# Kernel tuning notes

Measured on AMD Instinct MI355X. Metric: run time of the kernel, lower is better.

## Reference

```python
import jax, jax.numpy as jnp
import numpy as np

D = 1024
H = 16
FF = 4096
B = 8
N = 1024


def layer_norm(x, w, b, eps=1e-5):
    mu = jnp.mean(x, axis=-1, keepdims=True)
    var = jnp.var(x, axis=-1, keepdims=True)
    return (x - mu) * jax.lax.rsqrt(var + eps) * w + b


def setup_inputs() -> dict:
    key = jax.random.key(0)
    ks = jax.random.split(key, 8)
    s = 1.0 / np.sqrt(D)
    return {
        "x": jax.random.normal(ks[0], (B, N, D), dtype=jnp.float32),
        "attention_ids": jax.random.randint(ks[1], (B, N), 0, 2, dtype=jnp.int32),
        "norm1_w": jnp.ones((D,), jnp.float32),
        "norm1_b": jnp.zeros((D,), jnp.float32),
        "proj_in_w": jax.random.normal(ks[2], (3 * D, D), dtype=jnp.float32) * s,
        "proj_out_w": jax.random.normal(ks[3], (D, D), dtype=jnp.float32) * s,
        "proj_out_b": jnp.zeros((D,), jnp.float32),
        "norm2_w": jnp.ones((D,), jnp.float32),
        "norm2_b": jnp.zeros((D,), jnp.float32),
        "lin1_w": jax.random.normal(ks[4], (FF, D), dtype=jnp.float32) * s,
        "lin1_b": jnp.zeros((FF,), jnp.float32),
        "lin2_w": jax.random.normal(ks[5], (D, FF), dtype=jnp.float32) * (1.0 / np.sqrt(FF)),
        "lin2_b": jnp.zeros((D,), jnp.float32),
    }


def reference(x, attention_ids, norm1_w, norm1_b, proj_in_w, proj_out_w, proj_out_b,
              norm2_w, norm2_b, lin1_w, lin1_b, lin2_w, lin2_b):
    bs, ns, d = x.shape
    dh = d // H
    scale = dh ** -0.5

    # norm1 then attention with residual on the NORMED x (as in source)
    xn = layer_norm(x, norm1_w, norm1_b)
    qkv = jnp.einsum("bnd,ed->bne", xn, proj_in_w)          # [b,n,3d]
    qkv = qkv.reshape(bs, ns, 3, H, dh).transpose(2, 0, 3, 1, 4)
    q, k, v = qkv[0], qkv[1], qkv[2]                         # [b,h,n,dh]
    attn = jnp.einsum("bhqd,bhkd->bhqk", q, k)               # [b,h,n,n]
    mask_bias = (attention_ids.astype(x.dtype) * -1e9)[:, None, None, :]
    attn = jax.nn.softmax((attn + mask_bias) * scale, axis=-1)
    o = jnp.einsum("bhqk,bhkd->bhqd", attn, v)
    o = o.transpose(0, 2, 1, 3).reshape(bs, ns, d)
    o = jnp.einsum("bnd,ed->bne", o, proj_out_w) + proj_out_b
    x1 = o + xn

    # norm2 then FFN with residual on the NORMED x
    x2 = layer_norm(x1, norm2_w, norm2_b)
    h = jax.nn.gelu(jnp.einsum("bnd,fd->bnf", x2, lin1_w) + lin1_b, approximate=False)
    y = jnp.einsum("bnf,df->bnd", h, lin2_w) + lin2_b
    return y + x2
```

## Files before the change

kernel.cpp:

```cpp
#include <hip/hip_runtime.h>
#include <hip/hip_bf16.h>

#define B_ 8
#define N_ 1024
#define D_ 1024
#define H_ 16
#define FF_ 4096
#define TOK_ (B_*N_)

typedef __attribute__((ext_vector_type(8))) short bf16x8;
typedef __attribute__((ext_vector_type(4))) float f32x4;

typedef const __attribute__((address_space(1))) void* gc_ptr;
typedef __attribute__((address_space(3))) void* lp_ptr;

__device__ __forceinline__ short f2bf(float f) {
    unsigned u = __builtin_bit_cast(unsigned, f);
    u = (u + 0x7FFFu + ((u >> 16) & 1u)) >> 16;
    return (short)u;
}

__global__ __launch_bounds__(256)
void cvt_bf16(const float* __restrict__ in, short* __restrict__ outp) {
    const size_t i = ((size_t)blockIdx.x * 256 + threadIdx.x) * 4;
    const float4 v = *(const float4*)(in + i);
    short4 o;
    o.x = f2bf(v.x); o.y = f2bf(v.y); o.z = f2bf(v.z); o.w = f2bf(v.w);
    *(short4*)(outp + i) = o;
}

__global__ __launch_bounds__(256)
void ln_kernel(const float* __restrict__ in, const float* __restrict__ w,
               const float* __restrict__ bi, float* __restrict__ o32,
               short* __restrict__ obf) {
    const int row = blockIdx.x;
    const int tid = threadIdx.x;
    const float4 v = ((const float4*)(in + (size_t)row * D_))[tid];
    float s = v.x + v.y + v.z + v.w;
    float q = v.x * v.x + v.y * v.y + v.z * v.z + v.w * v.w;
#pragma unroll
    for (int off = 1; off < 64; off <<= 1) {
        s += __shfl_xor(s, off);
        q += __shfl_xor(q, off);
    }
    __shared__ float ss[4], sq[4];
    const int wave = tid >> 6, lane = tid & 63;
    if (lane == 0) { ss[wave] = s; sq[wave] = q; }
    __syncthreads();
    s = ss[0] + ss[1] + ss[2] + ss[3];
    q = sq[0] + sq[1] + sq[2] + sq[3];
    const float mu = s * (1.f / D_);
    const float var = q * (1.f / D_) - mu * mu;
    const float rs = rsqrtf(var + 1e-5f);
    const float4 wv = ((const float4*)w)[tid];
    const float4 bv = ((const float4*)bi)[tid];
    float4 o;
    o.x = (v.x - mu) * rs * wv.x + bv.x;
    o.y = (v.y - mu) * rs * wv.y + bv.y;
    o.z = (v.z - mu) * rs * wv.z + bv.z;
    o.w = (v.w - mu) * rs * wv.w + bv.w;
    ((float4*)(o32 + (size_t)row * D_))[tid] = o;
    short4 ob;
    ob.x = f2bf(o.x); ob.y = f2bf(o.y); ob.z = f2bf(o.z); ob.w = f2bf(o.w);
    *(short4*)(obf + (size_t)row * D_ + tid * 4) = ob;
}

template<int MODE>
__global__ __launch_bounds__(256, 2)
void gemm_bt(const short* __restrict__ A, const short* __restrict__ Bw,
             const float* __restrict__ bias, const float* __restrict__ res,
             void* __restrict__ outp, int M, int Nc, int K) {
    const int tid  = threadIdx.x;
    const int wave = tid >> 6;
    const int lane = tid & 63;
    const int m16  = lane & 15;
    const int quad = lane >> 4;
    const int wrow = (wave >> 1) * 64;
    const int wcol = (wave & 1) * 64;
    const int rowBase = blockIdx.y * 128;
    const int colBase = blockIdx.x * 128;

    __shared__ short sA[128 * 32];
    __shared__ short sB[128 * 32];

    f32x4 acc[4][4];
#pragma unroll
    for (int i = 0; i < 4; ++i)
#pragma unroll
        for (int j = 0; j < 4; ++j)
            acc[i][j] = {0.f, 0.f, 0.f, 0.f};

    const int r16 = lane >> 2;
    const int c4  = lane & 3;

    for (int kt = 0; kt < K; kt += 32) {
#pragma unroll
        for (int rep = 0; rep < 2; ++rep) {
            const int tr = rep * 64 + wave * 16;
            const short* ga = A  + (size_t)(rowBase + tr + r16) * K + kt + c4 * 8;
            const short* gb = Bw + (size_t)(colBase + tr + r16) * K + kt + c4 * 8;
            __builtin_amdgcn_global_load_lds((gc_ptr)ga, (lp_ptr)(sA + tr * 32), 16, 0, 0);
            __builtin_amdgcn_global_load_lds((gc_ptr)gb, (lp_ptr)(sB + tr * 32), 16, 0, 0);
        }
        asm volatile("s_waitcnt vmcnt(0)" ::: "memory");
        __syncthreads();

        bf16x8 af[4], bfr[4];
#pragma unroll
        for (int i = 0; i < 4; ++i)
            af[i] = *(const bf16x8*)(sA + (wrow + i * 16 + m16) * 32 + quad * 8);
#pragma unroll
        for (int j = 0; j < 4; ++j)
            bfr[j] = *(const bf16x8*)(sB + (wcol + j * 16 + m16) * 32 + quad * 8);
#pragma unroll
        for (int i = 0; i < 4; ++i)
#pragma unroll
            for (int j = 0; j < 4; ++j)
                acc[i][j] = __builtin_amdgcn_mfma_f32_16x16x32_bf16(af[i], bfr[j], acc[i][j], 0, 0, 0);
        __syncthreads();
    }

#pragma unroll
    for (int i = 0; i < 4; ++i) {
#pragma unroll
        for (int j = 0; j < 4; ++j) {
            const int col = colBase + wcol + j * 16 + m16;
#pragma unroll
            for (int r = 0; r < 4; ++r) {
                const int row = rowBase + wrow + i * 16 + quad * 4 + r;
                const float val = acc[i][j][r];
                if (MODE == 0) {
                    const int ci = col >> 10, hh = (col >> 6) & 15, dd = col & 63;
                    const int bb = row >> 10, nn = row & 1023;
                    size_t idx;
                    if (ci == 2)
                        idx = (size_t)2 * ((size_t)TOK_ * 1024) +
                              ((size_t)((bb * H_ + hh) * 64 + dd)) * N_ + nn;
                    else
                        idx = (size_t)ci * ((size_t)TOK_ * 1024) +
                              ((size_t)((bb * H_ + hh) * N_ + nn)) * 64 + dd;
                    ((short*)outp)[idx] = f2bf(val);
                } else if (MODE == 1) {
                    ((float*)outp)[(size_t)row * Nc + col] =
                        val + bias[col] + res[(size_t)row * Nc + col];
                } else {
                    const float t = val + bias[col];
                    const float g = 0.5f * t * (1.f + erff(t * 0.70710678118654752f));
                    ((short*)outp)[(size_t)row * Nc + col] = f2bf(g);
                }
            }
        }
    }
}

__global__ __launch_bounds__(256, 4)
void attn_kernel(const short* __restrict__ q, const short* __restrict__ k,
                 const short* __restrict__ vT, const int* __restrict__ ids,
                 short* __restrict__ outp) {
    const int tid  = threadIdx.x;
    const int wave = tid >> 6;
    const int lane = tid & 63;
    const int m    = lane & 15;
    const int quad = lane >> 4;
    const int b  = blockIdx.z;
    const int h  = blockIdx.y;
    const int q0 = blockIdx.x * 64;
    const size_t bh = ((size_t)b * H_ + h) * N_;

    __shared__ short Kb[2][4096];
    __shared__ short Vb[2][4096];
    __shared__ short Pl[4][16 * 40];

    const short* kbase  = k  + bh * 64;
    const short* vtbase = vT + bh * 64;
    const int* idrow = ids + b * N_;

    bf16x8 aq0, aq1;
    {
        const short* qp = q + (bh + q0 + wave * 16 + m) * 64;
        aq0 = *(const bf16x8*)(qp + quad * 8);
        aq1 = *(const bf16x8*)(qp + 32 + quad * 8);
    }

    const int l4 = lane >> 2, c3 = lane & 3;

    auto stage = [&](int t) {
        short* Kd = Kb[t & 1];
        short* Vd = Vb[t & 1];
        const int kt = t * 64;
        const int keyrow = 16 * wave + l4;
#pragma unroll
        for (int hh = 0; hh < 2; ++hh) {
            const short* gk = kbase + (size_t)(kt + keyrow) * 64 + hh * 32 + c3 * 8;
            __builtin_amdgcn_global_load_lds((gc_ptr)gk,
                (lp_ptr)(Kd + hh * 2048 + 512 * wave + lane * 8), 16, 0, 0);
        }
#pragma unroll
        for (int g = 0; g < 2; ++g) {
            const short* gv = vtbase + (size_t)keyrow * N_ + kt + g * 32 + c3 * 8;
            __builtin_amdgcn_global_load_lds((gc_ptr)gv,
                (lp_ptr)(Vd + g * 2048 + 512 * wave + lane * 8), 16, 0, 0);
        }
    };

    float plocal[4] = {0.f, 0.f, 0.f, 0.f};
    f32x4 o[4];
#pragma unroll
    for (int j = 0; j < 4; ++j) o[j] = {0.f, 0.f, 0.f, 0.f};

    short* pw = Pl[wave];

    stage(0);
    for (int t = 0; t < 16; ++t) {
        __syncthreads();
        if (t < 15) stage(t + 1);
        const short* Ks = Kb[t & 1];
        const short* Vs = Vb[t & 1];
        const int kt = t * 64;
#pragma unroll
        for (int g = 0; g < 2; ++g) {
            const float msk0 = -1e9f * (float)idrow[kt + g * 32 + m];
            const float msk1 = -1e9f * (float)idrow[kt + g * 32 + 16 + m];
            const bf16x8 b00 = *(const bf16x8*)(Ks + (g * 32 + m) * 32 + quad * 8);
            const bf16x8 b01 = *(const bf16x8*)(Ks + 2048 + (g * 32 + m) * 32 + quad * 8);
            const bf16x8 b10 = *(const bf16x8*)(Ks + (g * 32 + 16 + m) * 32 + quad * 8);
            const bf16x8 b11 = *(const bf16x8*)(Ks + 2048 + (g * 32 + 16 + m) * 32 + quad * 8);
            f32x4 s0 = {0.f, 0.f, 0.f, 0.f}, s1 = {0.f, 0.f, 0.f, 0.f};
            s0 = __builtin_amdgcn_mfma_f32_16x16x32_bf16(aq0, b00, s0, 0, 0, 0);
            s0 = __builtin_amdgcn_mfma_f32_16x16x32_bf16(aq1, b01, s0, 0, 0, 0);
            s1 = __builtin_amdgcn_mfma_f32_16x16x32_bf16(aq0, b10, s1, 0, 0, 0);
            s1 = __builtin_amdgcn_mfma_f32_16x16x32_bf16(aq1, b11, s1, 0, 0, 0);
#pragma unroll
            for (int r = 0; r < 4; ++r) {
                const float p0 = __expf((s0[r] + msk0) * 0.125f);
                const float p1 = __expf((s1[r] + msk1) * 0.125f);
                plocal[r] += p0 + p1;
                pw[(quad * 4 + r) * 40 + m]      = f2bf(p0);
                pw[(quad * 4 + r) * 40 + 16 + m] = f2bf(p1);
            }
            const bf16x8 pa = *(const bf16x8*)(pw + m * 40 + quad * 8);
#pragma unroll
            for (int j = 0; j < 4; ++j) {
                const bf16x8 bv = *(const bf16x8*)(Vs + g * 2048 + (j * 16 + m) * 32 + quad * 8);
                o[j] = __builtin_amdgcn_mfma_f32_16x16x32_bf16(pa, bv, o[j], 0, 0, 0);
            }
        }
    }

#pragma unroll
    for (int r = 0; r < 4; ++r) {
        float su = plocal[r];
        su += __shfl_xor(su, 1);
        su += __shfl_xor(su, 2);
        su += __shfl_xor(su, 4);
        su += __shfl_xor(su, 8);
        const float inv = 1.f / su;
        const int n = q0 + wave * 16 + quad * 4 + r;
        short* op = outp + ((size_t)(b * N_ + n)) * D_ + h * 64 + m;
#pragma unroll
        for (int j = 0; j < 4; ++j)
            op[j * 16] = f2bf(o[j][r] * inv);
    }
}

extern "C" void kernel_launch(void* const* d_in, const int* in_sizes, int n_in,
                              void* d_out, int out_size, void* d_ws, size_t ws_size,
                              hipStream_t stream) {
    const float* x   = (const float*)d_in[0];
    const int*   ids = (const int*)d_in[1];
    const float* n1w = (const float*)d_in[2];
    const float* n1b = (const float*)d_in[3];
    const float* win = (const float*)d_in[4];
    const float* wout= (const float*)d_in[5];
    const float* bout= (const float*)d_in[6];
    const float* n2w = (const float*)d_in[7];
    const float* n2b = (const float*)d_in[8];
    const float* w1  = (const float*)d_in[9];
    const float* b1  = (const float*)d_in[10];
    const float* w2  = (const float*)d_in[11];
    const float* b2  = (const float*)d_in[12];
    float* out = (float*)d_out;

    char* ws = (char*)d_ws;
    size_t off = 0;
    auto alloc = [&](size_t bytes) {
        char* p = ws + off;
        off += (bytes + 255) & ~(size_t)255;
        return p;
    };
    short* wq_b = (short*)alloc((size_t)3 * D_ * D_ * 2);
    short* wo_b = (short*)alloc((size_t)D_ * D_ * 2);
    short* w1_b = (short*)alloc((size_t)FF_ * D_ * 2);
    short* w2_b = (short*)alloc((size_t)D_ * FF_ * 2);
    float* xn32 = (float*)alloc((size_t)TOK_ * D_ * 4);
    short* xnb  = (short*)alloc((size_t)TOK_ * D_ * 2);
    short* qkv  = (short*)alloc((size_t)3 * TOK_ * D_ * 2);
    float* x2f  = (float*)alloc((size_t)TOK_ * D_ * 4);
    short* hbuf = (short*)alloc((size_t)TOK_ * FF_ * 2);
    short* attno = xnb;
    float* x1f   = (float*)qkv;
    short* x2b   = xnb;

    cvt_bf16<<<3 * D_ * D_ / 1024, 256, 0, stream>>>(win, wq_b);
    cvt_bf16<<<D_ * D_ / 1024, 256, 0, stream>>>(wout, wo_b);
    cvt_bf16<<<FF_ * D_ / 1024, 256, 0, stream>>>(w1, w1_b);
    cvt_bf16<<<FF_ * D_ / 1024, 256, 0, stream>>>(w2, w2_b);
    ln_kernel<<<TOK_, 256, 0, stream>>>(x, n1w, n1b, xn32, xnb);
    gemm_bt<0><<<dim3(3 * D_ / 128, TOK_ / 128), 256, 0, stream>>>(
        xnb, wq_b, nullptr, nullptr, qkv, TOK_, 3 * D_, D_);
    attn_kernel<<<dim3(N_ / 64, H_, B_), 256, 0, stream>>>(
        qkv, qkv + (size_t)TOK_ * D_, qkv + (size_t)2 * TOK_ * D_, ids, attno);
    gemm_bt<1><<<dim3(D_ / 128, TOK_ / 128), 256, 0, stream>>>(
        attno, wo_b, bout, xn32, x1f, TOK_, D_, D_);
    ln_kernel<<<TOK_, 256, 0, stream>>>(x1f, n2w, n2b, x2f, x2b);
    gemm_bt<2><<<dim3(FF_ / 128, TOK_ / 128), 256, 0, stream>>>(
        x2b, w1_b, b1, nullptr, hbuf, TOK_, FF_, D_);
    gemm_bt<1><<<dim3(D_ / 128, TOK_ / 128), 256, 0, stream>>>(
        hbuf, w2_b, b2, x2f, out, TOK_, D_, FF_);
}
```

Before: 560.5 us.

## Double-buffer GEMM LDS tiles and band-swizzle block order for L2 reuse

Splits the GEMM's shared-memory A and B tiles into two buffers, so the async global-to-LDS load of the next K-slice is issued while MFMAs run on the current one. This also drops one barrier per iteration. Separately, it remaps block indices into bands of 8 row-tiles so neighbouring blocks share A and B tiles in L2. The explicit vmcnt wait is removed, so correctness and overlap depend on compiler-inserted waits before the LDS reads. Those waits may be conservative and wait on the prefetch as well, or absent, which would be a race.

```diff
diff --git a/kernel.cpp b/kernel.cpp
--- a/kernel.cpp
+++ b/kernel.cpp
@@ -77,11 +77,17 @@
     const int quad = lane >> 4;
     const int wrow = (wave >> 1) * 64;
     const int wcol = (wave & 1) * 64;
-    const int rowBase = blockIdx.y * 128;
-    const int colBase = blockIdx.x * 128;
-
-    __shared__ short sA[128 * 32];
-    __shared__ short sB[128 * 32];
+
+    const int gx = gridDim.x;
+    const int lin = blockIdx.y * gx + blockIdx.x;
+    const int bandSz = gx * 8;
+    const int band = lin / bandSz;
+    const int rem  = lin - band * bandSz;
+    const int rowBase = (band * 8 + rem / gx) * 128;
+    const int colBase = (rem % gx) * 128;
+
+    __shared__ short sA[2][128 * 32];
+    __shared__ short sB[2][128 * 32];
 
     f32x4 acc[4][4];
 #pragma unroll
@@ -93,31 +99,40 @@
     const int r16 = lane >> 2;
     const int c4  = lane & 3;
 
-    for (int kt = 0; kt < K; kt += 32) {
+    auto stage = [&](int t) {
+        const int kt = t * 32;
+        short* dA = sA[t & 1];
+        short* dB = sB[t & 1];
 #pragma unroll
         for (int rep = 0; rep < 2; ++rep) {
             const int tr = rep * 64 + wave * 16;
             const short* ga = A  + (size_t)(rowBase + tr + r16) * K + kt + c4 * 8;
             const short* gb = Bw + (size_t)(colBase + tr + r16) * K + kt + c4 * 8;
-            __builtin_amdgcn_global_load_lds((gc_ptr)ga, (lp_ptr)(sA + tr * 32), 16, 0, 0);
-            __builtin_amdgcn_global_load_lds((gc_ptr)gb, (lp_ptr)(sB + tr * 32), 16, 0, 0);
-        }
-        asm volatile("s_waitcnt vmcnt(0)" ::: "memory");
+            __builtin_amdgcn_global_load_lds((gc_ptr)ga, (lp_ptr)(dA + tr * 32), 16, 0, 0);
+            __builtin_amdgcn_global_load_lds((gc_ptr)gb, (lp_ptr)(dB + tr * 32), 16, 0, 0);
+        }
+    };
+
+    const int T = K >> 5;
+    stage(0);
+    for (int t = 0; t < T; ++t) {
         __syncthreads();
+        if (t + 1 < T) stage(t + 1);
+        const short* cA = sA[t & 1];
+        const short* cB = sB[t & 1];
 
         bf16x8 af[4], bfr[4];
 #pragma unroll
         for (int i = 0; i < 4; ++i)
-            af[i] = *(const bf16x8*)(sA + (wrow + i * 16 + m16) * 32 + quad * 8);
+            af[i] = *(const bf16x8*)(cA + (wrow + i * 16 + m16) * 32 + quad * 8);
 #pragma unroll
         for (int j = 0; j < 4; ++j)
-            bfr[j] = *(const bf16x8*)(sB + (wcol + j * 16 + m16) * 32 + quad * 8);
+            bfr[j] = *(const bf16x8*)(cB + (wcol + j * 16 + m16) * 32 + quad * 8);
 #pragma unroll
         for (int i = 0; i < 4; ++i)
 #pragma unroll
             for (int j = 0; j < 4; ++j)
                 acc[i][j] = __builtin_amdgcn_mfma_f32_16x16x32_bf16(af[i], bfr[j], acc[i][j], 0, 0, 0);
-        __syncthreads();
     }
 
 #pragma unroll
```

After: 569.1 us. About the same (+1.5%).
